# Performance work log

Hardware: AMD Instinct MI355X
Metric: run time of the kernel (lower is better)

Reference implementation:

```python
import jax, jax.numpy as jnp
import numpy as np

H, N2, R = 512, 16, 32   # hidden_dim, state_dim//2, dt_rank=ceil(512/16)
B, L = 1, 4096


def setup_inputs() -> dict:
    key = jax.random.key(0)
    ks = jax.random.split(key, 7)
    u = jax.random.normal(ks[0], (B, L, H), dtype=jnp.float32)
    # Parameter initialization mirroring S4DKernel.__init__
    A_log = jnp.zeros((H, N2), jnp.float32)                      # log(ones)
    A_im = jnp.broadcast_to(jnp.arange(N2, dtype=jnp.float32), (H, N2)).copy()
    B_param = jax.random.normal(ks[1], (H, N2, 2), jnp.float32)
    C_param = jax.random.normal(ks[2], (H, N2, 2), jnp.float32)
    D = jax.random.normal(ks[3], (H,), jnp.float32)
    dt_w = jax.random.normal(ks[4], (H, R), jnp.float32) / np.sqrt(R)
    dt_min, dt_max, dt_floor = 1e-3, 0.1, 1e-4
    dt_init = jnp.exp(jax.random.uniform(ks[5], (H,), jnp.float32)
                      * (np.log(dt_max) - np.log(dt_floor)) + np.log(dt_floor))
    dt_init = jnp.maximum(dt_init, dt_min)
    dt_b = dt_init + jnp.log(-jnp.expm1(-dt_init))               # inverse-softplus init
    xproj_w = jax.random.normal(ks[6], (R, H), jnp.float32) / np.sqrt(H)
    return {"u": u, "A_log": A_log, "A_im": A_im, "B_param": B_param,
            "C_param": C_param, "D": D, "dt_w": dt_w, "dt_b": dt_b,
            "xproj_w": xproj_w}


def reference(u, A_log, A_im, B_param, C_param, D, dt_w, dt_b, xproj_w):
    # Complex continuous-time parameters
    A = -jnp.exp(A_log) + 1j * A_im                 # [H, N2]
    Bc = B_param[..., 0] + 1j * B_param[..., 1]     # [H, N2]
    Cc = C_param[..., 0] + 1j * C_param[..., 1]     # [H, N2]

    # dt path: x_proj_for_dt (no bias) -> dt_proj -> softplus
    dt_u = jnp.einsum('blh,rh->blr', u, xproj_w)                    # [B,L,R]
    dt = jax.nn.softplus(jnp.einsum('blr,hr->blh', dt_u, dt_w) + dt_b)  # [B,L,H]

    # ZOH discretization
    z = dt[..., None] * A                           # [B,L,H,N2] complex
    A_bar = jnp.exp(z)
    B_bar_div = jnp.where(jnp.abs(z) < 1e-4, 1.0 + z / 2, (jnp.exp(z) - 1.0) / z)
    ub = u[..., None].astype(A_bar.dtype) * B_bar_div * Bc          # [B,L,H,N2]

    # Parallel scan for h_k = A_k * h_{k-1} + u_k (first-order linear recurrence)
    def op(c1, c2):
        a1, b1 = c1
        a2, b2 = c2
        return a1 * a2, a2 * b1 + b2
    _, h = jax.lax.associative_scan(op, (A_bar, ub), axis=1)        # [B,L,H,N2]

    y = jnp.einsum('blhn,hn->blh', h, Cc) + u * D
    return y.real
```

## Files before the change

kernel.cpp:

```cpp
#include <hip/hip_runtime.h>

#define Hd 512
#define N2d 16
#define Rd 32
#define Ld 4096
#define NCHUNK 128
#define CLEN (Ld / NCHUNK)
#define NCH (Hd * N2d)
#define NGRP 16
#define NGROUPS (NCHUNK / NGRP)

__device__ __forceinline__ bool load_consts4(const float* A_log, const float* A_im,
        const float* B_param, int hnb,
        float* Are, float* Aim, float* BAr, float* BAi) {
    #pragma unroll
    for (int j = 0; j < 4; ++j) {
        int hn = hnb + j;
        Are[j] = -__expf(A_log[hn]);
        Aim[j] = A_im[hn];
        float Bre = B_param[2 * hn];
        float Bim = B_param[2 * hn + 1];
        float inv = __builtin_amdgcn_rcpf(Are[j] * Are[j] + Aim[j] * Aim[j]);
        BAr[j] = (Bre * Are[j] + Bim * Aim[j]) * inv;
        BAi[j] = (Bim * Are[j] - Bre * Aim[j]) * inv;
    }
    float d1 = Aim[1] - Aim[0], d2 = Aim[2] - Aim[1], d3 = Aim[3] - Aim[2];
    return (Are[1] == Are[0]) && (Are[2] == Are[0]) && (Are[3] == Are[0]) &&
           (d1 == d2) && (d2 == d3);
}

__global__ __launch_bounds__(256) void k_dt(const float* __restrict__ u,
                                            const float* __restrict__ xproj_w,
                                            const float* __restrict__ dt_w,
                                            const float* __restrict__ dt_b,
                                            float2* __restrict__ du_out) {
    __shared__ float u_s[8][Hd];
    __shared__ float dtu_s[8][Rd];
    const int t = threadIdx.x;
    const int l0 = blockIdx.x * 8;

    #pragma unroll
    for (int i = 0; i < 16; ++i) {
        int idx = t + i * 256;
        ((float*)u_s)[idx] = u[l0 * Hd + idx];
    }
    __syncthreads();

    const int r = t >> 3;
    const int j = t & 7;
    float part[8];
    #pragma unroll
    for (int l = 0; l < 8; ++l) part[l] = 0.f;
    for (int k = 0; k < 64; ++k) {
        float w = xproj_w[r * Hd + k * 8 + j];
        #pragma unroll
        for (int l = 0; l < 8; ++l) part[l] = fmaf(u_s[l][k * 8 + j], w, part[l]);
    }
    #pragma unroll
    for (int off = 1; off < 8; off <<= 1) {
        #pragma unroll
        for (int l = 0; l < 8; ++l) part[l] += __shfl_xor(part[l], off);
    }
    if (j == 0) {
        #pragma unroll
        for (int l = 0; l < 8; ++l) dtu_s[l][r] = part[l];
    }
    __syncthreads();

    #pragma unroll
    for (int hb = 0; hb < 2; ++hb) {
        int h = hb * 256 + t;
        float bias = dt_b[h];
        float acc[8];
        #pragma unroll
        for (int l = 0; l < 8; ++l) acc[l] = bias;
        #pragma unroll
        for (int rb = 0; rb < 8; ++rb) {
            float4 w = *(const float4*)&dt_w[h * Rd + rb * 4];
            #pragma unroll
            for (int l = 0; l < 8; ++l) {
                acc[l] = fmaf(dtu_s[l][rb * 4 + 0], w.x, acc[l]);
                acc[l] = fmaf(dtu_s[l][rb * 4 + 1], w.y, acc[l]);
                acc[l] = fmaf(dtu_s[l][rb * 4 + 2], w.z, acc[l]);
                acc[l] = fmaf(dtu_s[l][rb * 4 + 3], w.w, acc[l]);
            }
        }
        #pragma unroll
        for (int l = 0; l < 8; ++l) {
            float x = acc[l];
            float sp = fmaxf(x, 0.f) + log1pf(__expf(-fabsf(x)));
            float uv = u_s[l][h];
            float us = uv * __builtin_amdgcn_rcpf(fmaxf(sp, 1e-30f));
            du_out[(l0 + l) * Hd + h] = make_float2(sp, us);
        }
    }
}

__global__ __launch_bounds__(256) void k_chunk(const float2* __restrict__ du,
        const float* __restrict__ A_log, const float* __restrict__ A_im,
        const float* __restrict__ B_param, float4* __restrict__ PS) {
    const int t = threadIdx.x;
    const int q = t & 3;
    const int hh = blockIdx.y * 64 + (t >> 2);
    const int c = blockIdx.x;
    const int hnb = hh * N2d + q * 4;
    const int lbase = c * CLEN;

    float2 d0[16], d1[16];
    #pragma unroll
    for (int k = 0; k < 16; ++k) d0[k] = du[(lbase + k) * Hd + hh];
    #pragma unroll
    for (int k = 0; k < 16; ++k) d1[k] = du[(lbase + 16 + k) * Hd + hh];

    float Are[4], Aim[4], BAr[4], BAi[4];
    const bool fast = load_consts4(A_log, A_im, B_param, hnb, Are, Aim, BAr, BAi);
    float sr[4] = {0.f, 0.f, 0.f, 0.f}, si[4] = {0.f, 0.f, 0.f, 0.f};
    float sdt = 0.f;
    if (fast) {
        const float Are0 = Are[0], Aim0 = Aim[0], dA = Aim[1] - Aim[0];
        #pragma unroll
        for (int half = 0; half < 2; ++half) {
            #pragma unroll
            for (int k = 0; k < 16; ++k) {
                float2 d = half ? d1[k] : d0[k];
                float dtv = d.x, us = d.y;
                sdt += dtv;
                float er = __expf(dtv * Are0);
                float s0, c0, sd, cd;
                __sincosf(dtv * Aim0, &s0, &c0);
                __sincosf(dtv * dA, &sd, &cd);
                float ar = er * c0, ai = er * s0;
                #pragma unroll
                for (int jj = 0; jj < 4; ++jj) {
                    float gr = fmaf(ar, us, -us);
                    float gi = ai * us;
                    float nr = fmaf(ar, sr[jj], fmaf(-ai, si[jj], fmaf(gr, BAr[jj], -gi * BAi[jj])));
                    float ni = fmaf(ar, si[jj], fmaf( ai, sr[jj], fmaf(gr, BAi[jj],  gi * BAr[jj])));
                    sr[jj] = nr; si[jj] = ni;
                    if (jj < 3) {
                        float tr = fmaf(ar, cd, -ai * sd);
                        ai = fmaf(ai, cd, ar * sd);
                        ar = tr;
                    }
                }
            }
        }
    } else {
        #pragma unroll
        for (int half = 0; half < 2; ++half) {
            #pragma unroll
            for (int k = 0; k < 16; ++k) {
                float2 d = half ? d1[k] : d0[k];
                float dtv = d.x, us = d.y;
                sdt += dtv;
                #pragma unroll
                for (int jj = 0; jj < 4; ++jj) {
                    float er = __expf(dtv * Are[jj]);
                    float s, cc;
                    __sincosf(dtv * Aim[jj], &s, &cc);
                    float ar = er * cc, ai = er * s;
                    float gr = fmaf(ar, us, -us);
                    float gi = ai * us;
                    float nr = fmaf(ar, sr[jj], fmaf(-ai, si[jj], fmaf(gr, BAr[jj], -gi * BAi[jj])));
                    float ni = fmaf(ar, si[jj], fmaf( ai, sr[jj], fmaf(gr, BAi[jj],  gi * BAr[jj])));
                    sr[jj] = nr; si[jj] = ni;
                }
            }
        }
    }
    int base = c * NCH + hnb;
    #pragma unroll
    for (int jj = 0; jj < 4; ++jj) {
        float er = __expf(sdt * Are[jj]);
        float s, cc;
        __sincosf(sdt * Aim[jj], &s, &cc);
        PS[base + jj] = make_float4(er * cc, er * s, sr[jj], si[jj]);
    }
}

__global__ __launch_bounds__(256) void k_group(const float4* __restrict__ PS,
                                               float4* __restrict__ IP,
                                               float4* __restrict__ Gps) {
    int idx = blockIdx.x * 256 + threadIdx.x;
    int chain = idx & (NCH - 1);
    int g = idx >> 13;
    float pr = 1.f, pi = 0.f, hr = 0.f, hi = 0.f;
    #pragma unroll
    for (int half = 0; half < 2; ++half) {
        float4 ps[8];
        #pragma unroll
        for (int i = 0; i < 8; ++i)
            ps[i] = PS[(g * NGRP + half * 8 + i) * NCH + chain];
        #pragma unroll
        for (int i = 0; i < 8; ++i) {
            int c = g * NGRP + half * 8 + i;
            IP[c * NCH + chain] = make_float4(pr, pi, hr, hi);
            float nhr = fmaf(ps[i].x, hr, fmaf(-ps[i].y, hi, ps[i].z));
            float nhi = fmaf(ps[i].x, hi, fmaf( ps[i].y, hr, ps[i].w));
            float npr = fmaf(ps[i].x, pr, -ps[i].y * pi);
            float npi = fmaf(ps[i].x, pi,  ps[i].y * pr);
            hr = nhr; hi = nhi; pr = npr; pi = npi;
        }
    }
    Gps[g * NCH + chain] = make_float4(pr, pi, hr, hi);
}

__global__ __launch_bounds__(256) void k_gscan(const float4* __restrict__ Gps,
                                               float2* __restrict__ H0g) {
    int chain = blockIdx.x * 256 + threadIdx.x;
    float4 gp[NGROUPS];
    #pragma unroll
    for (int i = 0; i < NGROUPS; ++i)
        gp[i] = Gps[i * NCH + chain];
    float hr = 0.f, hi = 0.f;
    #pragma unroll
    for (int i = 0; i < NGROUPS; ++i) {
        H0g[i * NCH + chain] = make_float2(hr, hi);
        float nr = fmaf(gp[i].x, hr, fmaf(-gp[i].y, hi, gp[i].z));
        float ni = fmaf(gp[i].x, hi, fmaf( gp[i].y, hr, gp[i].w));
        hr = nr; hi = ni;
    }
}

__global__ __launch_bounds__(256) void k_scan(const float2* __restrict__ du,
        const float* __restrict__ A_log, const float* __restrict__ A_im,
        const float* __restrict__ B_param, const float* __restrict__ C_param,
        const float* __restrict__ Dp, const float4* __restrict__ IP,
        const float2* __restrict__ H0g, float* __restrict__ out) {
    const int t = threadIdx.x;
    const int q = t & 3;
    const int hh = blockIdx.y * 64 + (t >> 2);
    const int c = blockIdx.x;
    const int g = c / NGRP;
    const int hnb = hh * N2d + q * 4;
    const int lbase = c * CLEN;

    float2 d0[16], d1[16];
    #pragma unroll
    for (int k = 0; k < 16; ++k) d0[k] = du[(lbase + k) * Hd + hh];
    #pragma unroll
    for (int k = 0; k < 16; ++k) d1[k] = du[(lbase + 16 + k) * Hd + hh];

    float Are[4], Aim[4], BAr[4], BAi[4], Cre[4], Cim[4];
    const bool fast = load_consts4(A_log, A_im, B_param, hnb, Are, Aim, BAr, BAi);
    #pragma unroll
    for (int jj = 0; jj < 4; ++jj) {
        Cre[jj] = C_param[2 * (hnb + jj)];
        Cim[jj] = C_param[2 * (hnb + jj) + 1];
    }
    const float Dv = Dp[hh];

    float hr[4], hi[4];
    #pragma unroll
    for (int jj = 0; jj < 4; ++jj) {
        float4 ip = IP[c * NCH + hnb + jj];
        float2 hg = H0g[g * NCH + hnb + jj];
        hr[jj] = fmaf(ip.x, hg.x, fmaf(-ip.y, hg.y, ip.z));
        hi[jj] = fmaf(ip.x, hg.y, fmaf( ip.y, hg.x, ip.w));
    }

    if (fast) {
        const float Are0 = Are[0], Aim0 = Aim[0], dA = Aim[1] - Aim[0];
        #pragma unroll
        for (int half = 0; half < 2; ++half) {
            #pragma unroll
            for (int k = 0; k < 16; ++k) {
                int l = lbase + half * 16 + k;
                float2 d = half ? d1[k] : d0[k];
                float dtv = d.x, us = d.y;
                float er = __expf(dtv * Are0);
                float s0, c0, sd, cd;
                __sincosf(dtv * Aim0, &s0, &c0);
                __sincosf(dtv * dA, &sd, &cd);
                float ar = er * c0, ai = er * s0;
                float yv = 0.f;
                #pragma unroll
                for (int jj = 0; jj < 4; ++jj) {
                    float gr = fmaf(ar, us, -us);
                    float gi = ai * us;
                    float nr = fmaf(ar, hr[jj], fmaf(-ai, hi[jj], fmaf(gr, BAr[jj], -gi * BAi[jj])));
                    float ni = fmaf(ar, hi[jj], fmaf( ai, hr[jj], fmaf(gr, BAi[jj],  gi * BAr[jj])));
                    hr[jj] = nr; hi[jj] = ni;
                    yv = fmaf(nr, Cre[jj], fmaf(-ni, Cim[jj], yv));
                    if (jj < 3) {
                        float tr = fmaf(ar, cd, -ai * sd);
                        ai = fmaf(ai, cd, ar * sd);
                        ar = tr;
                    }
                }
                yv += __shfl_xor(yv, 1);
                yv += __shfl_xor(yv, 2);
                if (q == 0) out[l * Hd + hh] = fmaf(dtv * us, Dv, yv);
            }
        }
    } else {
        #pragma unroll
        for (int half = 0; half < 2; ++half) {
            #pragma unroll
            for (int k = 0; k < 16; ++k) {
                int l = lbase + half * 16 + k;
                float2 d = half ? d1[k] : d0[k];
                float dtv = d.x, us = d.y;
                float yv = 0.f;
                #pragma unroll
                for (int jj = 0; jj < 4; ++jj) {
                    float er = __expf(dtv * Are[jj]);
                    float s, cc;
                    __sincosf(dtv * Aim[jj], &s, &cc);
                    float ar = er * cc, ai = er * s;
                    float gr = fmaf(ar, us, -us);
                    float gi = ai * us;
                    float nr = fmaf(ar, hr[jj], fmaf(-ai, hi[jj], fmaf(gr, BAr[jj], -gi * BAi[jj])));
                    float ni = fmaf(ar, hi[jj], fmaf( ai, hr[jj], fmaf(gr, BAi[jj],  gi * BAr[jj])));
                    hr[jj] = nr; hi[jj] = ni;
                    yv = fmaf(nr, Cre[jj], fmaf(-ni, Cim[jj], yv));
                }
                yv += __shfl_xor(yv, 1);
                yv += __shfl_xor(yv, 2);
                if (q == 0) out[l * Hd + hh] = fmaf(dtv * us, Dv, yv);
            }
        }
    }
}

extern "C" void kernel_launch(void* const* d_in, const int* in_sizes, int n_in,
                              void* d_out, int out_size, void* d_ws, size_t ws_size,
                              hipStream_t stream) {
    const float* u        = (const float*)d_in[0];
    const float* A_log    = (const float*)d_in[1];
    const float* A_im     = (const float*)d_in[2];
    const float* B_param  = (const float*)d_in[3];
    const float* C_param  = (const float*)d_in[4];
    const float* Dp       = (const float*)d_in[5];
    const float* dt_w     = (const float*)d_in[6];
    const float* dt_b     = (const float*)d_in[7];
    const float* xproj_w  = (const float*)d_in[8];

    float2* du  = (float2*)d_ws;
    float4* PS  = (float4*)(du + (size_t)Ld * Hd);
    float4* IP  = PS + (size_t)NCHUNK * NCH;
    float4* Gps = IP + (size_t)NCHUNK * NCH;
    float2* H0g = (float2*)(Gps + (size_t)NGROUPS * NCH);
    float*  out = (float*)d_out;

    k_dt<<<Ld / 8, 256, 0, stream>>>(u, xproj_w, dt_w, dt_b, du);
    dim3 g2(NCHUNK, Hd / 64);
    k_chunk<<<g2, 256, 0, stream>>>(du, A_log, A_im, B_param, PS);
    k_group<<<(NCH * NGROUPS) / 256, 256, 0, stream>>>(PS, IP, Gps);
    k_gscan<<<NCH / 256, 256, 0, stream>>>(Gps, H0g);
    k_scan<<<g2, 256, 0, stream>>>(du, A_log, A_im, B_param, C_param, Dp,
                                   IP, H0g, out);
}
```

Measured before the change: 148.8 us.

## Emit zero-state chunk outputs in first pass and apply carry-in correction separately

The chunk pass now also computes each position's output under a zero initial state, along with the running dt sum, and writes both out. The second full recurrence pass is replaced by a per-(l,h) correction kernel. That kernel adds C·exp(A·T)·h0 using the cumulative dt and the chunk's carried-in state. This removes the recomputation of the whole scan in the final kernel. In exchange it writes and reads an extra L×H float2 buffer, and each output element reloads 16 states' IP/H0g/C values, with less reuse than before.

```diff
diff --git a/kernel.cpp b/kernel.cpp
--- a/kernel.cpp
+++ b/kernel.cpp
@@ -98,7 +98,9 @@
 
 __global__ __launch_bounds__(256) void k_chunk(const float2* __restrict__ du,
         const float* __restrict__ A_log, const float* __restrict__ A_im,
-        const float* __restrict__ B_param, float4* __restrict__ PS) {
+        const float* __restrict__ B_param, const float* __restrict__ C_param,
+        const float* __restrict__ Dp,
+        float4* __restrict__ PS, float2* __restrict__ y1T) {
     const int t = threadIdx.x;
     const int q = t & 3;
     const int hh = blockIdx.y * 64 + (t >> 2);
@@ -112,8 +114,15 @@
     #pragma unroll
     for (int k = 0; k < 16; ++k) d1[k] = du[(lbase + 16 + k) * Hd + hh];
 
-    float Are[4], Aim[4], BAr[4], BAi[4];
+    float Are[4], Aim[4], BAr[4], BAi[4], Cre[4], Cim[4];
     const bool fast = load_consts4(A_log, A_im, B_param, hnb, Are, Aim, BAr, BAi);
+    #pragma unroll
+    for (int jj = 0; jj < 4; ++jj) {
+        Cre[jj] = C_param[2 * (hnb + jj)];
+        Cim[jj] = C_param[2 * (hnb + jj) + 1];
+    }
+    const float Dv = Dp[hh];
+
     float sr[4] = {0.f, 0.f, 0.f, 0.f}, si[4] = {0.f, 0.f, 0.f, 0.f};
     float sdt = 0.f;
     if (fast) {
@@ -122,6 +131,7 @@
         for (int half = 0; half < 2; ++half) {
             #pragma unroll
             for (int k = 0; k < 16; ++k) {
+                int l = lbase + half * 16 + k;
                 float2 d = half ? d1[k] : d0[k];
                 float dtv = d.x, us = d.y;
                 sdt += dtv;
@@ -130,6 +140,7 @@
                 __sincosf(dtv * Aim0, &s0, &c0);
                 __sincosf(dtv * dA, &sd, &cd);
                 float ar = er * c0, ai = er * s0;
+                float yv = 0.f;
                 #pragma unroll
                 for (int jj = 0; jj < 4; ++jj) {
                     float gr = fmaf(ar, us, -us);
@@ -137,12 +148,16 @@
                     float nr = fmaf(ar, sr[jj], fmaf(-ai, si[jj], fmaf(gr, BAr[jj], -gi * BAi[jj])));
                     float ni = fmaf(ar, si[jj], fmaf( ai, sr[jj], fmaf(gr, BAi[jj],  gi * BAr[jj])));
                     sr[jj] = nr; si[jj] = ni;
+                    yv = fmaf(nr, Cre[jj], fmaf(-ni, Cim[jj], yv));
                     if (jj < 3) {
                         float tr = fmaf(ar, cd, -ai * sd);
                         ai = fmaf(ai, cd, ar * sd);
                         ar = tr;
                     }
                 }
+                yv += __shfl_xor(yv, 1);
+                yv += __shfl_xor(yv, 2);
+                if (q == 0) y1T[l * Hd + hh] = make_float2(fmaf(dtv * us, Dv, yv), sdt);
             }
         }
     } else {
@@ -150,9 +165,11 @@
         for (int half = 0; half < 2; ++half) {
             #pragma unroll
             for (int k = 0; k < 16; ++k) {
+                int l = lbase + half * 16 + k;
                 float2 d = half ? d1[k] : d0[k];
                 float dtv = d.x, us = d.y;
                 sdt += dtv;
+                float yv = 0.f;
                 #pragma unroll
                 for (int jj = 0; jj < 4; ++jj) {
                     float er = __expf(dtv * Are[jj]);
@@ -164,7 +181,11 @@
                     float nr = fmaf(ar, sr[jj], fmaf(-ai, si[jj], fmaf(gr, BAr[jj], -gi * BAi[jj])));
                     float ni = fmaf(ar, si[jj], fmaf( ai, sr[jj], fmaf(gr, BAi[jj],  gi * BAr[jj])));
                     sr[jj] = nr; si[jj] = ni;
+                    yv = fmaf(nr, Cre[jj], fmaf(-ni, Cim[jj], yv));
                 }
+                yv += __shfl_xor(yv, 1);
+                yv += __shfl_xor(yv, 2);
+                if (q == 0) y1T[l * Hd + hh] = make_float2(fmaf(dtv * us, Dv, yv), sdt);
             }
         }
     }
@@ -222,105 +243,74 @@
     }
 }
 
-__global__ __launch_bounds__(256) void k_scan(const float2* __restrict__ du,
+__global__ __launch_bounds__(256) void k_corr(const float2* __restrict__ y1T,
         const float* __restrict__ A_log, const float* __restrict__ A_im,
-        const float* __restrict__ B_param, const float* __restrict__ C_param,
-        const float* __restrict__ Dp, const float4* __restrict__ IP,
+        const float* __restrict__ C_param, const float4* __restrict__ IP,
         const float2* __restrict__ H0g, float* __restrict__ out) {
-    const int t = threadIdx.x;
-    const int q = t & 3;
-    const int hh = blockIdx.y * 64 + (t >> 2);
-    const int c = blockIdx.x;
-    const int g = c / NGRP;
-    const int hnb = hh * N2d + q * 4;
-    const int lbase = c * CLEN;
-
-    float2 d0[16], d1[16];
-    #pragma unroll
-    for (int k = 0; k < 16; ++k) d0[k] = du[(lbase + k) * Hd + hh];
-    #pragma unroll
-    for (int k = 0; k < 16; ++k) d1[k] = du[(lbase + 16 + k) * Hd + hh];
-
-    float Are[4], Aim[4], BAr[4], BAi[4], Cre[4], Cim[4];
-    const bool fast = load_consts4(A_log, A_im, B_param, hnb, Are, Aim, BAr, BAi);
-    #pragma unroll
-    for (int jj = 0; jj < 4; ++jj) {
-        Cre[jj] = C_param[2 * (hnb + jj)];
-        Cim[jj] = C_param[2 * (hnb + jj) + 1];
-    }
-    const float Dv = Dp[hh];
-
-    float hr[4], hi[4];
-    #pragma unroll
-    for (int jj = 0; jj < 4; ++jj) {
-        float4 ip = IP[c * NCH + hnb + jj];
-        float2 hg = H0g[g * NCH + hnb + jj];
-        hr[jj] = fmaf(ip.x, hg.x, fmaf(-ip.y, hg.y, ip.z));
-        hi[jj] = fmaf(ip.x, hg.y, fmaf( ip.y, hg.x, ip.w));
-    }
-
+    int gid = blockIdx.x * 256 + threadIdx.x;
+    int h = gid & (Hd - 1);
+    int l = gid >> 9;
+    int c = l >> 5;
+    int g = c >> 4;
+    int hn0 = h * N2d;
+
+    float2 yt = y1T[gid];
+    float T = yt.y;
+
+    float Are[N2d], Aim[N2d];
+    #pragma unroll
+    for (int n = 0; n < N2d; ++n) {
+        Are[n] = -__expf(A_log[hn0 + n]);
+        Aim[n] = A_im[hn0 + n];
+    }
+    float dA = Aim[1] - Aim[0];
+    bool fast = true;
+    #pragma unroll
+    for (int n = 1; n < N2d; ++n)
+        fast = fast && (Are[n] == Are[0]) && (Aim[n] - Aim[n - 1] == dA);
+
+    float corr = 0.f;
     if (fast) {
-        const float Are0 = Are[0], Aim0 = Aim[0], dA = Aim[1] - Aim[0];
-        #pragma unroll
-        for (int half = 0; half < 2; ++half) {
-            #pragma unroll
-            for (int k = 0; k < 16; ++k) {
-                int l = lbase + half * 16 + k;
-                float2 d = half ? d1[k] : d0[k];
-                float dtv = d.x, us = d.y;
-                float er = __expf(dtv * Are0);
-                float s0, c0, sd, cd;
-                __sincosf(dtv * Aim0, &s0, &c0);
-                __sincosf(dtv * dA, &sd, &cd);
-                float ar = er * c0, ai = er * s0;
-                float yv = 0.f;
-                #pragma unroll
-                for (int jj = 0; jj < 4; ++jj) {
-                    float gr = fmaf(ar, us, -us);
-                    float gi = ai * us;
-                    float nr = fmaf(ar, hr[jj], fmaf(-ai, hi[jj], fmaf(gr, BAr[jj], -gi * BAi[jj])));
-                    float ni = fmaf(ar, hi[jj], fmaf( ai, hr[jj], fmaf(gr, BAi[jj],  gi * BAr[jj])));
-                    hr[jj] = nr; hi[jj] = ni;
-                    yv = fmaf(nr, Cre[jj], fmaf(-ni, Cim[jj], yv));
-                    if (jj < 3) {
-                        float tr = fmaf(ar, cd, -ai * sd);
-                        ai = fmaf(ai, cd, ar * sd);
-                        ar = tr;
-                    }
-                }
-                yv += __shfl_xor(yv, 1);
-                yv += __shfl_xor(yv, 2);
-                if (q == 0) out[l * Hd + hh] = fmaf(dtv * us, Dv, yv);
+        float er = __expf(Are[0] * T);
+        float s0, c0, sd, cd;
+        __sincosf(Aim[0] * T, &s0, &c0);
+        __sincosf(dA * T, &sd, &cd);
+        float ar = er * c0, ai = er * s0;
+        #pragma unroll
+        for (int n = 0; n < N2d; ++n) {
+            float4 ip = IP[c * NCH + hn0 + n];
+            float2 hg = H0g[g * NCH + hn0 + n];
+            float h0r = fmaf(ip.x, hg.x, fmaf(-ip.y, hg.y, ip.z));
+            float h0i = fmaf(ip.x, hg.y, fmaf( ip.y, hg.x, ip.w));
+            float Cr = C_param[2 * (hn0 + n)];
+            float Ci = C_param[2 * (hn0 + n) + 1];
+            float wr = fmaf(Cr, h0r, -Ci * h0i);
+            float wi = fmaf(Cr, h0i,  Ci * h0r);
+            corr = fmaf(ar, wr, fmaf(-ai, wi, corr));
+            if (n < N2d - 1) {
+                float tr = fmaf(ar, cd, -ai * sd);
+                ai = fmaf(ai, cd, ar * sd);
+                ar = tr;
             }
         }
     } else {
         #pragma unroll
-        for (int half = 0; half < 2; ++half) {
-            #pragma unroll
-            for (int k = 0; k < 16; ++k) {
-                int l = lbase + half * 16 + k;
-                float2 d = half ? d1[k] : d0[k];
-                float dtv = d.x, us = d.y;
-                float yv = 0.f;
-                #pragma unroll
-                for (int jj = 0; jj < 4; ++jj) {
-                    float er = __expf(dtv * Are[jj]);
-                    float s, cc;
-                    __sincosf(dtv * Aim[jj], &s, &cc);
-                    float ar = er * cc, ai = er * s;
-                    float gr = fmaf(ar, us, -us);
-                    float gi = ai * us;
-                    float nr = fmaf(ar, hr[jj], fmaf(-ai, hi[jj], fmaf(gr, BAr[jj], -gi * BAi[jj])));
-                    float ni = fmaf(ar, hi[jj], fmaf( ai, hr[jj], fmaf(gr, BAi[jj],  gi * BAr[jj])));
-                    hr[jj] = nr; hi[jj] = ni;
-                    yv = fmaf(nr, Cre[jj], fmaf(-ni, Cim[jj], yv));
-                }
-                yv += __shfl_xor(yv, 1);
-                yv += __shfl_xor(yv, 2);
-                if (q == 0) out[l * Hd + hh] = fmaf(dtv * us, Dv, yv);
-            }
-        }
-    }
+        for (int n = 0; n < N2d; ++n) {
+            float4 ip = IP[c * NCH + hn0 + n];
+            float2 hg = H0g[g * NCH + hn0 + n];
+            float h0r = fmaf(ip.x, hg.x, fmaf(-ip.y, hg.y, ip.z));
+            float h0i = fmaf(ip.x, hg.y, fmaf( ip.y, hg.x, ip.w));
+            float Cr = C_param[2 * (hn0 + n)];
+            float Ci = C_param[2 * (hn0 + n) + 1];
+            float wr = fmaf(Cr, h0r, -Ci * h0i);
+            float wi = fmaf(Cr, h0i,  Ci * h0r);
+            float er = __expf(Are[n] * T);
+            float s, cc;
+            __sincosf(Aim[n] * T, &s, &cc);
+            corr = fmaf(er * cc, wr, fmaf(-er * s, wi, corr));
+        }
+    }
+    out[gid] = yt.x + corr;
 }
 
 extern "C" void kernel_launch(void* const* d_in, const int* in_sizes, int n_in,
@@ -341,13 +331,14 @@
     float4* IP  = PS + (size_t)NCHUNK * NCH;
     float4* Gps = IP + (size_t)NCHUNK * NCH;
     float2* H0g = (float2*)(Gps + (size_t)NGROUPS * NCH);
+    float2* y1T = H0g + (size_t)NGROUPS * NCH;
     float*  out = (float*)d_out;
 
     k_dt<<<Ld / 8, 256, 0, stream>>>(u, xproj_w, dt_w, dt_b, du);
     dim3 g2(NCHUNK, Hd / 64);
-    k_chunk<<<g2, 256, 0, stream>>>(du, A_log, A_im, B_param, PS);
+    k_chunk<<<g2, 256, 0, stream>>>(du, A_log, A_im, B_param, C_param, Dp, PS, y1T);
     k_group<<<(NCH * NGROUPS) / 256, 256, 0, stream>>>(PS, IP, Gps);
     k_gscan<<<NCH / 256, 256, 0, stream>>>(Gps, H0g);
-    k_scan<<<g2, 256, 0, stream>>>(du, A_log, A_im, B_param, C_param, Dp,
-                                   IP, H0g, out);
-}
+    k_corr<<<(Ld * Hd) / 256, 256, 0, stream>>>(y1T, A_log, A_im, C_param,
+                                                IP, H0g, out);
+}
```

Measured after the change: 282.7 us. 90.0% more time.
